# Kernel tuning notes

Measured on AMD Instinct MI355X. Metric: run time of the kernel, lower is better.

Reference implementation:

```python
import jax, jax.numpy as jnp
import numpy as np

C, H, L, P = 256, 8, 4, 4   # embed_dim, num_heads, num_levels, num_points
B, N = 2, 16384             # batch, total queries
SHAPES = [(64, 64), (128, 128), (256, 256), (512, 512)]  # last = base (finest)


def setup_inputs() -> dict:
    key = jax.random.key(0)
    ks = jax.random.split(key, 16)
    d = {}
    d["query"] = jax.random.normal(ks[0], (N, C), jnp.float32)
    d["query_offsets"] = jnp.array([0, N // 2], jnp.int32)
    base_h, base_w = SHAPES[-1]
    # un-normalized reference points in finest-level pixel coords, kept away from edges
    d["reference_points"] = (
        jax.random.uniform(ks[1], (N, 2), jnp.float32)
        * jnp.array([base_h - 16, base_w - 16], jnp.float32) + 8.0
    )
    for l, (h, w) in enumerate(SHAPES):
        d[f"value{l}"] = jax.random.normal(ks[2 + l], (B, h, w, C), jnp.float32) * 0.1
    d["W_off"] = jax.random.normal(ks[6], (C, H * L * P * 2), jnp.float32) * 0.01
    d["b_off"] = jax.random.normal(ks[7], (H * L * P * 2,), jnp.float32) * 2.0
    d["W_attn"] = jax.random.normal(ks[8], (C, H * L * P), jnp.float32) * 0.02
    d["b_attn"] = jnp.zeros((H * L * P,), jnp.float32)
    d["W_val"] = jax.random.normal(ks[9], (C, C), jnp.float32) * (1.0 / np.sqrt(C))
    d["b_val"] = jnp.zeros((C,), jnp.float32)
    d["W_out"] = jax.random.normal(ks[10], (C, C), jnp.float32) * (1.0 / np.sqrt(C))
    d["b_out"] = jnp.zeros((C,), jnp.float32)
    return d


def _bilinear_sample(v, loc, batch_id):
    """v: [B,h,w,H,dh] per-head feature map; loc: [N,H,P,2] (i,j) pixel coords;
    batch_id: [N]. Returns [N,H,P,dh]. Mirrors sparse_interp: shift by 0.5,
    clamp_min 0, floor, frac weights, max-index clamp."""
    h, w = v.shape[1], v.shape[2]
    sc = jnp.maximum(loc - 0.5, 0.0)
    i0 = jnp.floor(sc).astype(jnp.int32)
    frac = sc - jnp.floor(sc)
    b = batch_id[:, None, None]                 # [N,1,1]
    hidx = jnp.arange(H)[None, :, None]         # [1,H,1]

    def g(di, dj):
        ii = jnp.clip(i0[..., 0] + di, 0, h - 1)
        jj = jnp.clip(i0[..., 1] + dj, 0, w - 1)
        return v[b, ii, jj, hidx]               # [N,H,P,dh]

    dw = frac[..., 0:1]  # down weight
    rw = frac[..., 1:2]  # right weight
    uw, lw = 1.0 - dw, 1.0 - rw
    return uw * lw * g(0, 0) + uw * rw * g(0, 1) + dw * lw * g(1, 0) + dw * rw * g(1, 1)


def reference(query, query_offsets, reference_points, value0, value1, value2, value3,
              W_off, b_off, W_attn, b_attn, W_val, b_val, W_out, b_out):
    values = [value0, value1, value2, value3]
    n = query.shape[0]
    dh = C // H
    # sampling offsets and attention weights from query
    off = (query @ W_off + b_off).reshape(n, H, L, P, 2)
    attn = jax.nn.softmax((query @ W_attn + b_attn).reshape(n, H, L * P), axis=-1)
    attn = attn.reshape(n, H, L, P)
    base = jnp.asarray(values[-1].shape[1:3], jnp.float32)
    # which batch element each query belongs to
    batch_id = jnp.searchsorted(query_offsets, jnp.arange(n), side="right") - 1
    sampled = []
    for l, v in enumerate(values):
        hl, wl = v.shape[1], v.shape[2]
        scaler = jnp.array([hl, wl], jnp.float32) / base
        loc = (reference_points[:, None, None, :] + off[:, :, l]) * scaler  # [N,H,P,2]
        # value_proj: per-pixel 1x1 linear, then split heads
        vp = (v @ W_val + b_val).reshape(v.shape[0], hl, wl, H, dh)
        sampled.append(_bilinear_sample(vp, loc, batch_id))
    sampled = jnp.stack(sampled, axis=2)        # [N,H,L,P,dh]
    out = (sampled * attn[..., None]).sum(axis=(2, 3)).reshape(n, C)
    return out @ W_out + b_out
```

## Files before the change

### kernel.cpp

```cpp
#include <hip/hip_runtime.h>


typedef float f32x4 __attribute__((ext_vector_type(4)));
typedef _Float16 f16;
typedef f16 f16x8 __attribute__((ext_vector_type(8)));
typedef f16 f16x4 __attribute__((ext_vector_type(4)));

template<int M>
__global__ __launch_bounds__(M)
void gemm_rb(const float* __restrict__ X, const float* __restrict__ W,
             const float* __restrict__ bias, float* __restrict__ Y) {
    __shared__ float xt[32 * 256];
    const int tid = threadIdx.x;
    const long row0 = (long)blockIdx.x * 32;
    const float4* src = (const float4*)(X + row0 * 256);
    float4* dst4 = (float4*)xt;
    for (int i = tid; i < 32 * 64; i += M) dst4[i] = src[i];
    __syncthreads();

    constexpr int CG = M / 4;
    const int cg = tid % CG, qg = tid / CG;
    const int c0 = cg * 4, q0 = qg * 8;

    f32x4 acc[8];
#pragma unroll
    for (int qi = 0; qi < 8; ++qi) acc[qi] = (f32x4){0.f, 0.f, 0.f, 0.f};

    for (int k4 = 0; k4 < 64; ++k4) {
        f32x4 w[4];
#pragma unroll
        for (int r = 0; r < 4; ++r)
            w[r] = *(const f32x4*)&W[(size_t)(k4 * 4 + r) * M + c0];
        f32x4 xv[8];
#pragma unroll
        for (int qi = 0; qi < 8; ++qi)
            xv[qi] = *(const f32x4*)&xt[(q0 + qi) * 256 + k4 * 4];
#pragma unroll
        for (int qi = 0; qi < 8; ++qi) {
            f32x4 a = acc[qi];
            const f32x4 x = xv[qi];
            a.x = fmaf(x.x, w[0].x, a.x); a.y = fmaf(x.x, w[0].y, a.y);
            a.z = fmaf(x.x, w[0].z, a.z); a.w = fmaf(x.x, w[0].w, a.w);
            a.x = fmaf(x.y, w[1].x, a.x); a.y = fmaf(x.y, w[1].y, a.y);
            a.z = fmaf(x.y, w[1].z, a.z); a.w = fmaf(x.y, w[1].w, a.w);
            a.x = fmaf(x.z, w[2].x, a.x); a.y = fmaf(x.z, w[2].y, a.y);
            a.z = fmaf(x.z, w[2].z, a.z); a.w = fmaf(x.z, w[2].w, a.w);
            a.x = fmaf(x.w, w[3].x, a.x); a.y = fmaf(x.w, w[3].y, a.y);
            a.z = fmaf(x.w, w[3].z, a.z); a.w = fmaf(x.w, w[3].w, a.w);
            acc[qi] = a;
        }
    }

    const f32x4 bv = *(const f32x4*)&bias[c0];
#pragma unroll
    for (int qi = 0; qi < 8; ++qi) {
        f32x4 o = acc[qi];
        o.x += bv.x; o.y += bv.y; o.z += bv.z; o.w += bv.w;
        *(f32x4*)&Y[(size_t)(row0 + q0 + qi) * M + c0] = o;
    }
}

__global__ __launch_bounds__(384)
void gemm_qproj(const float* __restrict__ X,
                const float* __restrict__ W_off, const float* __restrict__ b_off,
                const float* __restrict__ W_attn, const float* __restrict__ b_attn,
                float* __restrict__ Y1, float* __restrict__ Y2) {
    __shared__ float xt[32 * 260];
    const int tid = threadIdx.x;
    const long row0 = (long)blockIdx.x * 32;
    const float4* src = (const float4*)(X + row0 * 256);
    for (int i = tid; i < 32 * 64; i += 384) {
        const int r = i >> 6, c4 = i & 63;
        *(float4*)(xt + r * 260 + c4 * 4) = src[i];
    }
    __syncthreads();

    const int cg = tid % 96, qg = tid / 96;
    const int c0 = cg * 4, q0 = qg * 8;
    const bool off_part = (c0 < 256);
    const float* Wp = off_part ? (W_off + c0) : (W_attn + (c0 - 256));
    const float* bp = off_part ? (b_off + c0) : (b_attn + (c0 - 256));
    const int ldW = off_part ? 256 : 128;
    float* Yp = off_part ? (Y1 + c0) : (Y2 + (c0 - 256));

    f32x4 acc[8];
#pragma unroll
    for (int qi = 0; qi < 8; ++qi) acc[qi] = (f32x4){0.f, 0.f, 0.f, 0.f};

    for (int k4 = 0; k4 < 64; ++k4) {
        f32x4 w[4];
#pragma unroll
        for (int r = 0; r < 4; ++r)
            w[r] = *(const f32x4*)&Wp[(size_t)(k4 * 4 + r) * ldW];
        f32x4 xv[8];
#pragma unroll
        for (int qi = 0; qi < 8; ++qi)
            xv[qi] = *(const f32x4*)&xt[(q0 + qi) * 260 + k4 * 4];
#pragma unroll
        for (int qi = 0; qi < 8; ++qi) {
            f32x4 a = acc[qi];
            const f32x4 x = xv[qi];
            a.x = fmaf(x.x, w[0].x, a.x); a.y = fmaf(x.x, w[0].y, a.y);
            a.z = fmaf(x.x, w[0].z, a.z); a.w = fmaf(x.x, w[0].w, a.w);
            a.x = fmaf(x.y, w[1].x, a.x); a.y = fmaf(x.y, w[1].y, a.y);
            a.z = fmaf(x.y, w[1].z, a.z); a.w = fmaf(x.y, w[1].w, a.w);
            a.x = fmaf(x.z, w[2].x, a.x); a.y = fmaf(x.z, w[2].y, a.y);
            a.z = fmaf(x.z, w[2].z, a.z); a.w = fmaf(x.z, w[2].w, a.w);
            a.x = fmaf(x.w, w[3].x, a.x); a.y = fmaf(x.w, w[3].y, a.y);
            a.z = fmaf(x.w, w[3].z, a.z); a.w = fmaf(x.w, w[3].w, a.w);
            acc[qi] = a;
        }
    }

    const f32x4 bv = *(const f32x4*)bp;
#pragma unroll
    for (int qi = 0; qi < 8; ++qi) {
        f32x4 o = acc[qi];
        o.x += bv.x; o.y += bv.y; o.z += bv.z; o.w += bv.w;
        *(f32x4*)&Yp[(size_t)(row0 + q0 + qi) * ldW] = o;
    }
}

#define NBINS 4096

__device__ __forceinline__ int bin_of(float ri, float rj) {
    int bi = (int)ri >> 3, bj = (int)rj >> 3;
    bi = min(63, max(0, bi)); bj = min(63, max(0, bj));
    return bi * 64 + bj;
}

__global__ void bin_hist(const float* __restrict__ refp, int* __restrict__ hist, int N) {
    const int n = blockIdx.x * blockDim.x + threadIdx.x;
    if (n < N) atomicAdd(&hist[bin_of(refp[2 * n], refp[2 * n + 1])], 1);
}

__global__ __launch_bounds__(256)
void bin_scan(const int* __restrict__ hist, int* __restrict__ binptr) {
    __shared__ int part[256];
    const int t = threadIdx.x;
    int vals[16], excl[16], run = 0;
#pragma unroll
    for (int i = 0; i < 16; ++i) { vals[i] = hist[t * 16 + i]; }
#pragma unroll
    for (int i = 0; i < 16; ++i) { excl[i] = run; run += vals[i]; }
    part[t] = run;
    __syncthreads();
    int off = 0;
    for (int i = 0; i < t; ++i) off += part[i];
#pragma unroll
    for (int i = 0; i < 16; ++i) binptr[t * 16 + i] = off + excl[i];
}

__global__ void bin_scatter(const float* __restrict__ refp, int* __restrict__ binptr,
                            int* __restrict__ perm, int N) {
    const int n = blockIdx.x * blockDim.x + threadIdx.x;
    if (n < N) {
        const int b = bin_of(refp[2 * n], refp[2 * n + 1]);
        const int pos = atomicAdd(&binptr[b], 1);
        perm[pos] = n;
    }
}

__global__ __launch_bounds__(256)
void prep_wvF(const float* __restrict__ W, f16* __restrict__ wvF) {
    const int k = blockIdx.x, n = threadIdx.x;
    const int ks = k >> 5, kg = (k >> 3) & 3, j = k & 7;
    const int tile = n >> 4, l15 = n & 15;
    const int lane = (kg << 4) | l15;
    wvF[((size_t)(ks * 16 + tile) * 512) + lane * 8 + j] = (f16)W[(size_t)k * 256 + n];
}

__global__ __launch_bounds__(256)
void proj_val_all(const float* __restrict__ v0, const float* __restrict__ v1,
                  const float* __restrict__ v2, const float* __restrict__ v3,
                  const f16* __restrict__ wvF, const float* __restrict__ bval,
                  f16* __restrict__ vp0, f16* __restrict__ vp1,
                  f16* __restrict__ vp2, f16* __restrict__ vp3) {
    __shared__ f16 At[32][264];
    const int tid = threadIdx.x;

    const int bid = blockIdx.x;
    const float* V; f16* VP; long px0;
    if (bid < 256)        { V = v0; VP = vp0; px0 = (long)bid * 32; }
    else if (bid < 1280)  { V = v1; VP = vp1; px0 = (long)(bid - 256) * 32; }
    else if (bid < 5376)  { V = v2; VP = vp2; px0 = (long)(bid - 1280) * 32; }
    else                  { V = v3; VP = vp3; px0 = (long)(bid - 5376) * 32; }

    {
        const int wv_ = tid >> 6, ln_ = tid & 63;
#pragma unroll
        for (int i = 0; i < 8; ++i) {
            const int px = wv_ + i * 4;
            const float4 v4 = *(const float4*)(V + (px0 + px) * 256 + ln_ * 4);
            f16x4 h4 = {(f16)v4.x, (f16)v4.y, (f16)v4.z, (f16)v4.w};
            *(f16x4*)(&At[px][ln_ * 4]) = h4;
        }
    }
    __syncthreads();

    const int wave = tid >> 6, lane = tid & 63;
    const int l15 = lane & 15, kg = lane >> 4;

    f32x4 acc[2][4];
#pragma unroll
    for (int a = 0; a < 2; ++a)
#pragma unroll
        for (int b = 0; b < 4; ++b) acc[a][b] = (f32x4){0.f, 0.f, 0.f, 0.f};

#pragma unroll
    for (int ks = 0; ks < 8; ++ks) {
        f16x8 wf[4];
#pragma unroll
        for (int ct = 0; ct < 4; ++ct)
            wf[ct] = *(const f16x8*)(wvF + ((size_t)(ks * 16 + wave * 4 + ct) * 512) + lane * 8);
        f16x8 vf[2];
#pragma unroll
        for (int pt = 0; pt < 2; ++pt)
            vf[pt] = *(const f16x8*)(&At[pt * 16 + l15][ks * 32 + kg * 8]);
#pragma unroll
        for (int pt = 0; pt < 2; ++pt)
#pragma unroll
            for (int ct = 0; ct < 4; ++ct)
                acc[pt][ct] = __builtin_amdgcn_mfma_f32_16x16x32_f16(wf[ct], vf[pt], acc[pt][ct], 0, 0, 0);
    }

    __syncthreads();

    const int ch0 = wave * 64;
#pragma unroll
    for (int ct = 0; ct < 4; ++ct) {
        const int chb = ch0 + ct * 16 + kg * 4;
        const float4 bv = *(const float4*)(bval + chb);
#pragma unroll
        for (int pt = 0; pt < 2; ++pt) {
            f16x4 o = {(f16)(acc[pt][ct].x + bv.x), (f16)(acc[pt][ct].y + bv.y),
                       (f16)(acc[pt][ct].z + bv.z), (f16)(acc[pt][ct].w + bv.w)};
            *(f16x4*)(&At[pt * 16 + l15][chb]) = o;
        }
    }
    __syncthreads();

    f16* dst = VP + (size_t)px0 * 256;
#pragma unroll
    for (int i = 0; i < 4; ++i) {
        const int e0 = (i * 256 + tid) * 8;
        const int px = e0 >> 8;
        const int ch = e0 & 255;
        *(f16x8*)(dst + e0) = *(const f16x8*)(&At[px][ch]);
    }
}

#define GQPB 8
__global__ __launch_bounds__(256)
void gather_vp(const float* __restrict__ offs_all,
               const float* __restrict__ logits_all,
               const float* __restrict__ refpts,
               const int* __restrict__ qoff, int n_off,
               const int* __restrict__ perm,
               const f16* __restrict__ vp0, const f16* __restrict__ vp1,
               const f16* __restrict__ vp2, const f16* __restrict__ vp3,
               float* __restrict__ val_out) {
    __shared__ float sOff[GQPB][256];
    __shared__ float sAttn[GQPB][128];
    __shared__ int   sQ[GQPB];
    const int tid = threadIdx.x;

    const int bid = blockIdx.x;
    const int cpx = gridDim.x >> 3;
    const int swz = (bid & 7) * cpx + (bid >> 3);
    const int n0p = swz * GQPB;

    if (tid < GQPB) sQ[tid] = perm[n0p + tid];
    __syncthreads();

    {
        const int q = tid >> 5, i = tid & 31;
        const int nq = sQ[q];
        ((f32x4*)sOff[q])[i]      = ((const f32x4*)(offs_all + (size_t)nq * 256))[i];
        ((f32x4*)sOff[q])[i + 32] = ((const f32x4*)(offs_all + (size_t)nq * 256))[i + 32];
        ((f32x4*)sAttn[q])[i]     = ((const f32x4*)(logits_all + (size_t)nq * 128))[i];
    }
    __syncthreads();

    if (tid < GQPB * 8) {
        float* row = &sAttn[tid >> 3][(tid & 7) * 16];
        float m = -1e30f;
#pragma unroll
        for (int i = 0; i < 16; ++i) m = fmaxf(m, row[i]);
        float s = 0.f;
#pragma unroll
        for (int i = 0; i < 16; ++i) { const float e = expf(row[i] - m); row[i] = e; s += e; }
        const float inv = 1.f / s;
#pragma unroll
        for (int i = 0; i < 16; ++i) row[i] *= inv;
    }
    __syncthreads();

    const int q = tid >> 5, h = (tid >> 2) & 7, s = tid & 3;
    const int n = sQ[q];
    int b = 0;
    for (int i = 1; i < n_off; ++i) if (n >= qoff[i]) b = i;
    const float ri = refpts[2 * n], rj = refpts[2 * n + 1];
    const int choff = h * 32 + s * 8;

    float acc[8];
#pragma unroll
    for (int j = 0; j < 8; ++j) acc[j] = 0.f;

#pragma unroll
    for (int l = 0; l < 4; ++l) {
        const int hw = (l == 0 ? 64 : (l == 1 ? 128 : (l == 2 ? 256 : 512)));
        const float sc = (float)hw * (1.0f / 512.0f);
        const f16* vbl = (l == 0 ? vp0 : (l == 1 ? vp1 : (l == 2 ? vp2 : vp3)));
        const f16* __restrict__ vb = vbl + (size_t)b * ((size_t)hw * hw * 256) + choff;

#pragma unroll
        for (int pp = 0; pp < 4; pp += 2) {
            int   o[8];
            float wgt[8];
#pragma unroll
            for (int pq = 0; pq < 2; ++pq) {
                const int p = pp + pq;
                const int oi = ((h * 4 + l) * 4 + p) * 2;
                const float fi = (ri + sOff[q][oi]) * sc;
                const float fj = (rj + sOff[q][oi + 1]) * sc;
                const float a = sAttn[q][(h * 4 + l) * 4 + p];
                const float sci = fmaxf(fi - 0.5f, 0.f);
                const float scj = fmaxf(fj - 0.5f, 0.f);
                const float fl_i = floorf(sci), fl_j = floorf(scj);
                const int i0 = (int)fl_i, j0 = (int)fl_j;
                const float fri = sci - fl_i, frj = scj - fl_j;
                const int i0c = min(i0, hw - 1), i1c = min(i0 + 1, hw - 1);
                const int j0c = min(j0, hw - 1), j1c = min(j0 + 1, hw - 1);
                const float uw = 1.f - fri, lw = 1.f - frj;
                o[pq * 4 + 0] = (i0c * hw + j0c) << 8;
                o[pq * 4 + 1] = (i0c * hw + j1c) << 8;
                o[pq * 4 + 2] = (i1c * hw + j0c) << 8;
                o[pq * 4 + 3] = (i1c * hw + j1c) << 8;
                wgt[pq * 4 + 0] = uw * lw * a;
                wgt[pq * 4 + 1] = uw * frj * a;
                wgt[pq * 4 + 2] = fri * lw * a;
                wgt[pq * 4 + 3] = fri * frj * a;
            }

            f16x8 buf[8];
#pragma unroll
            for (int k = 0; k < 8; ++k)
                buf[k] = *(const f16x8*)(vb + (size_t)o[k]);
            asm volatile("" : "+v"(buf[0]), "+v"(buf[1]), "+v"(buf[2]), "+v"(buf[3]),
                              "+v"(buf[4]), "+v"(buf[5]), "+v"(buf[6]), "+v"(buf[7])
                            :: "memory");
#pragma unroll
            for (int k = 0; k < 8; ++k) {
                const float wv = wgt[k];
#pragma unroll
                for (int j = 0; j < 8; ++j)
                    acc[j] = fmaf(wv, (float)buf[k][j], acc[j]);
            }
        }
    }

    float* op = val_out + (size_t)n * 256 + choff;
    *(f32x4*)op       = (f32x4){acc[0], acc[1], acc[2], acc[3]};
    *(f32x4*)(op + 4) = (f32x4){acc[4], acc[5], acc[6], acc[7]};
}

extern "C" void kernel_launch(void* const* d_in, const int* in_sizes, int n_in,
                              void* d_out, int out_size, void* d_ws, size_t ws_size,
                              hipStream_t stream) {
    const float* query  = (const float*)d_in[0];
    const int*   qoff   = (const int*)d_in[1];
    const float* refp   = (const float*)d_in[2];
    const float* v0     = (const float*)d_in[3];
    const float* v1     = (const float*)d_in[4];
    const float* v2     = (const float*)d_in[5];
    const float* v3     = (const float*)d_in[6];
    const float* W_off  = (const float*)d_in[7];
    const float* b_off  = (const float*)d_in[8];
    const float* W_attn = (const float*)d_in[9];
    const float* b_attn = (const float*)d_in[10];
    const float* W_val  = (const float*)d_in[11];
    const float* b_val  = (const float*)d_in[12];
    const float* W_out  = (const float*)d_in[13];
    const float* b_out  = (const float*)d_in[14];
    float* out = (float*)d_out;

    const int N = in_sizes[0] / 256;
    const int n_off = in_sizes[1];

    float* P1off  = (float*)d_ws;
    float* P1attn = P1off + (size_t)N * 256;
    int*   hist   = (int*)(P1attn + (size_t)N * 128);
    int*   binptr = hist + NBINS;
    int*   perm   = binptr + NBINS;

    const int M0 = 2 * 64 * 64, M1 = 2 * 128 * 128, M2 = 2 * 256 * 256, M3 = 2 * 512 * 512;
    const size_t base_b = (size_t)N * 256 * 4 + (size_t)N * 128 * 4 + (size_t)(2 * NBINS + N) * 4;

    hipMemsetAsync(hist, 0, NBINS * sizeof(int), stream);
    bin_hist<<<(N + 255) / 256, 256, 0, stream>>>(refp, hist, N);
    bin_scan<<<1, 256, 0, stream>>>(hist, binptr);
    bin_scatter<<<(N + 255) / 256, 256, 0, stream>>>(refp, binptr, perm, N);

    gemm_qproj<<<N / 32, 384, 0, stream>>>(query, W_off, b_off, W_attn, b_attn,
                                           P1off, P1attn);

    f16* wvF = (f16*)((char*)d_ws + base_b);
    f16* vp0 = wvF + 65536;
    f16* vp1 = vp0 + (size_t)M0 * 256;
    f16* vp2 = vp1 + (size_t)M1 * 256;
    f16* vp3 = vp2 + (size_t)M2 * 256;

    prep_wvF<<<256, 256, 0, stream>>>(W_val, wvF);
    proj_val_all<<<21760, 256, 0, stream>>>(v0, v1, v2, v3, wvF, b_val,
                                            vp0, vp1, vp2, vp3);

    gather_vp<<<N / GQPB, 256, 0, stream>>>(P1off, P1attn, refp, qoff, n_off,
                                            perm, vp0, vp1, vp2, vp3, out);

    gemm_rb<256><<<N / 32, 256, 0, stream>>>(out, W_out, b_out, out);
}
```

Baseline: 543.3 us.

## Store projected values head-major and split bilinear corners across lane pairs

The value projection now writes its fp16 output in a head-major layout [B][H][h*w][32], so each head's feature map is contiguous and the bilinear corner fetches for one head touch smaller, denser regions. The gather kernel halves queries per block and assigns two lanes per channel slice, each handling one column of the bilinear corners, then reduces them with a cross-lane shuffle. This is meant to improve cache locality and raise parallelism in the gather. It costs an extra shuffle and duplicated offset math per lane, and the grid size must match the new GQPB.

```diff
diff --git a/kernel.cpp b/kernel.cpp
--- a/kernel.cpp
+++ b/kernel.cpp
@@ -180,11 +180,11 @@
     const int tid = threadIdx.x;
 
     const int bid = blockIdx.x;
-    const float* V; f16* VP; long px0;
-    if (bid < 256)        { V = v0; VP = vp0; px0 = (long)bid * 32; }
-    else if (bid < 1280)  { V = v1; VP = vp1; px0 = (long)(bid - 256) * 32; }
-    else if (bid < 5376)  { V = v2; VP = vp2; px0 = (long)(bid - 1280) * 32; }
-    else                  { V = v3; VP = vp3; px0 = (long)(bid - 5376) * 32; }
+    const float* V; f16* VP; long px0; long hwsq;
+    if (bid < 256)        { V = v0; VP = vp0; px0 = (long)bid * 32;          hwsq = 4096;   }
+    else if (bid < 1280)  { V = v1; VP = vp1; px0 = (long)(bid - 256) * 32;  hwsq = 16384;  }
+    else if (bid < 5376)  { V = v2; VP = vp2; px0 = (long)(bid - 1280) * 32; hwsq = 65536;  }
+    else                  { V = v3; VP = vp3; px0 = (long)(bid - 5376) * 32; hwsq = 262144; }
 
     {
         const int wv_ = tid >> 6, ln_ = tid & 63;
@@ -240,17 +240,22 @@
     }
     __syncthreads();
 
-    f16* dst = VP + (size_t)px0 * 256;
+    const long bt = (px0 >= hwsq) ? 1 : 0;
+    const long pxb = px0 - bt * hwsq;
+    f16* base = VP + (size_t)bt * hwsq * 256;
 #pragma unroll
     for (int i = 0; i < 4; ++i) {
-        const int e0 = (i * 256 + tid) * 8;
-        const int px = e0 >> 8;
-        const int ch = e0 & 255;
-        *(f16x8*)(dst + e0) = *(const f16x8*)(&At[px][ch]);
-    }
-}
-
-#define GQPB 8
+        const int c2 = i * 256 + tid;
+        const int hh = c2 >> 7;
+        const int rem = c2 & 127;
+        const int px = rem >> 2;
+        const int sub = rem & 3;
+        *(f16x8*)(base + (size_t)hh * hwsq * 32 + (pxb + px) * 32 + sub * 8) =
+            *(const f16x8*)(&At[px][hh * 32 + sub * 8]);
+    }
+}
+
+#define GQPB 4
 __global__ __launch_bounds__(256)
 void gather_vp(const float* __restrict__ offs_all,
                const float* __restrict__ logits_all,
@@ -274,11 +279,10 @@
     __syncthreads();
 
     {
-        const int q = tid >> 5, i = tid & 31;
+        const int q = tid >> 6, i = tid & 63;
         const int nq = sQ[q];
-        ((f32x4*)sOff[q])[i]      = ((const f32x4*)(offs_all + (size_t)nq * 256))[i];
-        ((f32x4*)sOff[q])[i + 32] = ((const f32x4*)(offs_all + (size_t)nq * 256))[i + 32];
-        ((f32x4*)sAttn[q])[i]     = ((const f32x4*)(logits_all + (size_t)nq * 128))[i];
+        ((f32x4*)sOff[q])[i] = ((const f32x4*)(offs_all + (size_t)nq * 256))[i];
+        if (i < 32) ((f32x4*)sAttn[q])[i] = ((const f32x4*)(logits_all + (size_t)nq * 128))[i];
     }
     __syncthreads();
 
@@ -296,12 +300,13 @@
     }
     __syncthreads();
 
-    const int q = tid >> 5, h = (tid >> 2) & 7, s = tid & 3;
+    const int q = tid >> 6, h = (tid >> 3) & 7;
+    const int l8 = tid & 7, s = l8 & 3, jc = l8 >> 2;
     const int n = sQ[q];
     int b = 0;
     for (int i = 1; i < n_off; ++i) if (n >= qoff[i]) b = i;
     const float ri = refpts[2 * n], rj = refpts[2 * n + 1];
-    const int choff = h * 32 + s * 8;
+    const int s8 = s * 8;
 
     float acc[8];
 #pragma unroll
@@ -310,59 +315,62 @@
 #pragma unroll
     for (int l = 0; l < 4; ++l) {
         const int hw = (l == 0 ? 64 : (l == 1 ? 128 : (l == 2 ? 256 : 512)));
+        const long hwsq = (long)hw * hw;
         const float sc = (float)hw * (1.0f / 512.0f);
         const f16* vbl = (l == 0 ? vp0 : (l == 1 ? vp1 : (l == 2 ? vp2 : vp3)));
-        const f16* __restrict__ vb = vbl + (size_t)b * ((size_t)hw * hw * 256) + choff;
-
-#pragma unroll
-        for (int pp = 0; pp < 4; pp += 2) {
-            int   o[8];
-            float wgt[8];
-#pragma unroll
-            for (int pq = 0; pq < 2; ++pq) {
-                const int p = pp + pq;
-                const int oi = ((h * 4 + l) * 4 + p) * 2;
-                const float fi = (ri + sOff[q][oi]) * sc;
-                const float fj = (rj + sOff[q][oi + 1]) * sc;
-                const float a = sAttn[q][(h * 4 + l) * 4 + p];
-                const float sci = fmaxf(fi - 0.5f, 0.f);
-                const float scj = fmaxf(fj - 0.5f, 0.f);
-                const float fl_i = floorf(sci), fl_j = floorf(scj);
-                const int i0 = (int)fl_i, j0 = (int)fl_j;
-                const float fri = sci - fl_i, frj = scj - fl_j;
-                const int i0c = min(i0, hw - 1), i1c = min(i0 + 1, hw - 1);
-                const int j0c = min(j0, hw - 1), j1c = min(j0 + 1, hw - 1);
-                const float uw = 1.f - fri, lw = 1.f - frj;
-                o[pq * 4 + 0] = (i0c * hw + j0c) << 8;
-                o[pq * 4 + 1] = (i0c * hw + j1c) << 8;
-                o[pq * 4 + 2] = (i1c * hw + j0c) << 8;
-                o[pq * 4 + 3] = (i1c * hw + j1c) << 8;
-                wgt[pq * 4 + 0] = uw * lw * a;
-                wgt[pq * 4 + 1] = uw * frj * a;
-                wgt[pq * 4 + 2] = fri * lw * a;
-                wgt[pq * 4 + 3] = fri * frj * a;
+        const f16* __restrict__ vb = vbl + (size_t)b * hwsq * 256 + (size_t)h * hwsq * 32 + s8;
+
+        int   a0[4], a1[4];
+        float w0v[4], w1v[4];
+#pragma unroll
+        for (int p = 0; p < 4; ++p) {
+            const int oi = ((h * 4 + l) * 4 + p) * 2;
+            const float fi = (ri + sOff[q][oi]) * sc;
+            const float fj = (rj + sOff[q][oi + 1]) * sc;
+            const float a = sAttn[q][(h * 4 + l) * 4 + p];
+            const float sci = fmaxf(fi - 0.5f, 0.f);
+            const float scj = fmaxf(fj - 0.5f, 0.f);
+            const float fl_i = floorf(sci), fl_j = floorf(scj);
+            const int i0 = (int)fl_i, j0 = (int)fl_j;
+            const float fri = sci - fl_i, frj = scj - fl_j;
+            const int i0c = min(i0, hw - 1), i1c = min(i0 + 1, hw - 1);
+            const int j0c = min(j0, hw - 1), j1c = min(j0 + 1, hw - 1);
+            const float uw = 1.f - fri, lw = 1.f - frj;
+            const int jsel = jc ? j1c : j0c;
+            a0[p] = (i0c * hw + jsel) * 32;
+            a1[p] = (i1c * hw + jsel) * 32;
+            w0v[p] = (jc ? uw * frj : uw * lw) * a;
+            w1v[p] = (jc ? fri * frj : fri * lw) * a;
+        }
+
+        f16x8 buf[8];
+#pragma unroll
+        for (int p = 0; p < 4; ++p) {
+            buf[2 * p]     = *(const f16x8*)(vb + (size_t)a0[p]);
+            buf[2 * p + 1] = *(const f16x8*)(vb + (size_t)a1[p]);
+        }
+        asm volatile("" : "+v"(buf[0]), "+v"(buf[1]), "+v"(buf[2]), "+v"(buf[3]),
+                          "+v"(buf[4]), "+v"(buf[5]), "+v"(buf[6]), "+v"(buf[7])
+                        :: "memory");
+#pragma unroll
+        for (int p = 0; p < 4; ++p) {
+            const float wa = w0v[p], wb = w1v[p];
+#pragma unroll
+            for (int j = 0; j < 8; ++j) {
+                acc[j] = fmaf(wa, (float)buf[2 * p][j], acc[j]);
+                acc[j] = fmaf(wb, (float)buf[2 * p + 1][j], acc[j]);
             }
-
-            f16x8 buf[8];
-#pragma unroll
-            for (int k = 0; k < 8; ++k)
-                buf[k] = *(const f16x8*)(vb + (size_t)o[k]);
-            asm volatile("" : "+v"(buf[0]), "+v"(buf[1]), "+v"(buf[2]), "+v"(buf[3]),
-                              "+v"(buf[4]), "+v"(buf[5]), "+v"(buf[6]), "+v"(buf[7])
-                            :: "memory");
-#pragma unroll
-            for (int k = 0; k < 8; ++k) {
-                const float wv = wgt[k];
-#pragma unroll
-                for (int j = 0; j < 8; ++j)
-                    acc[j] = fmaf(wv, (float)buf[k][j], acc[j]);
-            }
-        }
-    }
-
-    float* op = val_out + (size_t)n * 256 + choff;
-    *(f32x4*)op       = (f32x4){acc[0], acc[1], acc[2], acc[3]};
-    *(f32x4*)(op + 4) = (f32x4){acc[4], acc[5], acc[6], acc[7]};
+        }
+    }
+
+#pragma unroll
+    for (int j = 0; j < 8; ++j) acc[j] += __shfl_xor(acc[j], 4);
+
+    if (jc == 0) {
+        float* op = val_out + (size_t)n * 256 + h * 32 + s8;
+        *(f32x4*)op       = (f32x4){acc[0], acc[1], acc[2], acc[3]};
+        *(f32x4*)(op + 4) = (f32x4){acc[4], acc[5], acc[6], acc[7]};
+    }
 }
 
 extern "C" void kernel_launch(void* const* d_in, const int* in_sizes, int n_in,
```

After: 463.1 us. -14.8%, faster.
